# Kernel optimization log

Measured on AMD Instinct MI355X. Metric: run time of the kernel, lower is better.

## Reference

```python
import jax, jax.numpy as jnp
import numpy as np

B, LA, LB = 16, 2048, 2048
DA, DB, DH = 768, 512, 512
EPS = 1e-5


def _layer_norm(x, g, b):
    mu = jnp.mean(x, axis=-1, keepdims=True)
    var = jnp.var(x, axis=-1, keepdims=True)
    return (x - mu) * jax.lax.rsqrt(var + EPS) * g + b


def setup_inputs() -> dict:
    key = jax.random.key(0)
    ks = jax.random.split(key, 12)
    s = lambda d: 1.0 / np.sqrt(d)
    return {
        "z_a": jax.random.normal(ks[0], (B, LA, DA), jnp.float32),
        "z_b": jax.random.normal(ks[1], (B, LB, DB), jnp.float32),
        "Wa": jax.random.uniform(ks[2], (DA, DH), jnp.float32, -s(DA), s(DA)),
        "ba": jnp.zeros((DH,), jnp.float32),
        "Wb": jax.random.uniform(ks[3], (DB, DH), jnp.float32, -s(DB), s(DB)),
        "bb": jnp.zeros((DH,), jnp.float32),
        "W_co": jax.random.normal(ks[4], (DH, DH), jnp.float32),
        "Woa": jax.random.uniform(ks[5], (DH, DA), jnp.float32, -s(DH), s(DH)),
        "boa": jnp.zeros((DA,), jnp.float32),
        "Wob": jax.random.uniform(ks[6], (DH, DB), jnp.float32, -s(DH), s(DH)),
        "bob": jnp.zeros((DB,), jnp.float32),
        "ga": jnp.ones((DA,), jnp.float32),
        "beta_a": jnp.zeros((DA,), jnp.float32),
        "gb": jnp.ones((DB,), jnp.float32),
        "beta_b": jnp.zeros((DB,), jnp.float32),
    }


def reference(z_a, z_b, Wa, ba, Wb, bb, W_co, Woa, boa, Wob, bob, ga, beta_a, gb, beta_b):
    # projections to shared hidden space
    h_a = jnp.einsum('bld,dh->blh', z_a, Wa) + ba          # (B, LA, DH)
    h_b = jnp.einsum('bld,dh->blh', z_b, Wb) + bb          # (B, LB, DH)
    # bilinear tanh co-attention scores
    C = jnp.tanh(jnp.einsum('bih,hk,bjk->bij', h_a, W_co, h_b))  # (B, LA, LB)
    attn_a = jax.nn.softmax(C, axis=-1)                    # rows: over LB
    attn_b = jax.nn.softmax(C.transpose(0, 2, 1), axis=-1) # cols: over LA
    h_a_co = jnp.einsum('bij,bjh->bih', attn_a, h_b)       # (B, LA, DH)
    h_b_co = jnp.einsum('bji,bih->bjh', attn_b, h_a)       # (B, LB, DH)
    z_a_co = jnp.einsum('blh,hd->bld', h_a_co, Woa) + boa
    z_b_co = jnp.einsum('blh,hd->bld', h_b_co, Wob) + bob
    z_a_out = _layer_norm(z_a + z_a_co, ga, beta_a)
    z_b_out = _layer_norm(z_b + z_b_co, gb, beta_b)
    return (z_a_out, z_b_out)
```

## Files before the change

### kernel.cpp

```cpp
#include <hip/hip_runtime.h>
#include <stdint.h>

typedef short bf16x8 __attribute__((ext_vector_type(8)));
typedef float f32x16 __attribute__((ext_vector_type(16)));

#define BM 256
#define BN 256
#define BK 64
#define ABUF_U 16384
#define BUF_U  32768

#define AS1 __attribute__((address_space(1)))
#define AS3 __attribute__((address_space(3)))

__device__ __forceinline__ ushort f2bf(float x) {
    uint32_t u = __float_as_uint(x);
    u += 0x7FFFu + ((u >> 16) & 1u);
    return (ushort)(u >> 16);
}
__device__ __forceinline__ float bf2f(ushort u) {
    return __uint_as_float((uint)u << 16);
}

__device__ __forceinline__ void gload16(const void* g, void* l) {
    __builtin_amdgcn_global_load_lds((const AS1 void*)g, (AS3 void*)l, 16, 0, 0);
}

#define ISSUE2(kt, buf, i0)                                                          \
    do {                                                                             \
        gload16(((i0) < 4 ? Ap : Bp) + goff[i0] + (kt), smem + (buf)*BUF_U + loff[i0]); \
        gload16((((i0)+1) < 4 ? Ap : Bp) + goff[(i0)+1] + (kt), smem + (buf)*BUF_U + loff[(i0)+1]); \
    } while (0)

template<int MODE, bool HAS_BIAS, bool WRITE_T>
__global__ __launch_bounds__(512, 2)
void gemm_bt(const ushort* __restrict__ Aptr_, const ushort* __restrict__ Bptr_,
             void* __restrict__ Cptr_, ushort* __restrict__ CTptr_,
             const float* __restrict__ bias, const ushort* __restrict__ resid_,
             float* __restrict__ rsum_, float* __restrict__ csum_,
             const float* __restrict__ scale_,
             const ushort* __restrict__ Aptr2_, const ushort* __restrict__ Bptr2_,
             void* __restrict__ Cptr2_, const float* __restrict__ scale2_, int zsplit,
             int M, int N, int K, int lda, int ldb, int ldc,
             long sA, long sB, long sC, long sCT, long sSum,
             int ldct, int rbshift)
{
    extern __shared__ ushort smem[];

    const int gx = gridDim.x, gy = gridDim.y;
    const int nwg = gx * gy * (int)gridDim.z;
    int flat = ((int)blockIdx.z * gy + (int)blockIdx.y) * gx + (int)blockIdx.x;
    {
        const int q8 = nwg >> 3, r8 = nwg & 7;
        const int xcd = flat & 7, loc = flat >> 3;
        flat = (xcd < r8 ? xcd * (q8 + 1) : r8 * (q8 + 1) + (xcd - r8) * q8) + loc;
    }
    const int z   = flat / (gx * gy);
    const int rem = flat - z * (gx * gy);
    const int m0  = (rem % gx) * BM;
    const int n0  = (rem / gx) * BN;

    const bool sec = (z >= zsplit);
    const int  zl  = sec ? z - zsplit : z;

    const int tid  = threadIdx.x;
    const int lane = tid & 63;
    const int wave = tid >> 6;
    const int wr   = wave >> 2;
    const int wcn  = wave & 3;
    const int lr   = lane & 31, lh = lane >> 5;

    const ushort* Ap = (sec ? Aptr2_ : Aptr_) + (long)zl * sA;
    const ushort* Bp = (sec ? Bptr2_ : Bptr_) + (long)zl * sB;

    long goff[8]; int loff[8];
    #pragma unroll
    for (int u = 0; u < 4; ++u) {
        const int li  = u * 512 + tid;
        const int row = li >> 3;
        const int gck = (li & 7) ^ (row & 7);
        goff[u]     = (long)(m0 + row) * lda + gck * 8;
        loff[u]     = li * 8;
        goff[u + 4] = (long)(n0 + row) * ldb + gck * 8;
        loff[u + 4] = ABUF_U + li * 8;
    }

    f32x16 acc[4][2] = {};

    const int nk = K / BK;
    ISSUE2(0, 0, 0); ISSUE2(0, 0, 2); ISSUE2(0, 0, 4); ISSUE2(0, 0, 6);

    for (int t = 0; t < nk; ++t) {
        const int cur = t & 1, nxt = cur ^ 1;
        const ushort* As = smem + cur * BUF_U;
        const ushort* Bs = As + ABUF_U;
        const bool pf = (t + 1 < nk);
        const int kt1 = (t + 1) * BK;

        if (pf) {
            ISSUE2(kt1, nxt, 0);
            asm volatile("s_waitcnt vmcnt(2)" ::: "memory");
        } else {
            asm volatile("s_waitcnt vmcnt(0)" ::: "memory");
        }
        __builtin_amdgcn_s_barrier();

        #pragma unroll
        for (int kk = 0; kk < 4; ++kk) {
            bf16x8 af[4], bfv[2];
            #pragma unroll
            for (int tm = 0; tm < 4; ++tm) {
                const int row = wr * 128 + tm * 32 + lr;
                const int ck  = (kk * 2 + lh) ^ (row & 7);
                af[tm] = *(const bf16x8*)&As[row * BK + ck * 8];
            }
            #pragma unroll
            for (int tn = 0; tn < 2; ++tn) {
                const int row = wcn * 64 + tn * 32 + lr;
                const int ck  = (kk * 2 + lh) ^ (row & 7);
                bfv[tn] = *(const bf16x8*)&Bs[row * BK + ck * 8];
            }
            if (pf) {
                if (kk == 0)      ISSUE2(kt1, nxt, 2);
                else if (kk == 1) ISSUE2(kt1, nxt, 4);
                else if (kk == 2) ISSUE2(kt1, nxt, 6);
            }
            #pragma unroll
            for (int tm = 0; tm < 4; ++tm)
                #pragma unroll
                for (int tn = 0; tn < 2; ++tn)
                    acc[tm][tn] = __builtin_amdgcn_mfma_f32_32x32x16_bf16(
                        af[tm], bfv[tn], acc[tm][tn], 0, 0, 0);
        }

        asm volatile("s_waitcnt lgkmcnt(0)" ::: "memory");
        __builtin_amdgcn_s_barrier();
    }

    const int colb0 = n0 + wcn * 64 + lr;
    const int rowbw = m0 + wr * 128 + 4 * lh;

    if constexpr (MODE == 3) {
        ushort* Cp = (ushort*)Cptr_;
        #pragma unroll
        for (int tm = 0; tm < 4; ++tm)
            #pragma unroll
            for (int tn = 0; tn < 2; ++tn) {
                const int col = colb0 + tn * 32;
                const float bv = bias[col];
                #pragma unroll
                for (int q = 0; q < 4; ++q)
                    #pragma unroll
                    for (int s = 0; s < 4; ++s) {
                        const int row = rowbw + tm * 32 + q * 8 + s;
                        const long idx = (long)row * ldc + col;
                        Cp[idx] = f2bf(acc[tm][tn][q * 4 + s] + bv + bf2f(resid_[idx]));
                    }
            }
    } else if constexpr (MODE == 0) {
        ushort* Cp = (ushort*)Cptr_ + zl * sC;
        #pragma unroll
        for (int tm = 0; tm < 4; ++tm)
            #pragma unroll
            for (int tn = 0; tn < 2; ++tn) {
                const int col = colb0 + tn * 32;
                const float bv = HAS_BIAS ? bias[col] : 0.f;
                ushort us[16];
                #pragma unroll
                for (int rr = 0; rr < 16; ++rr) us[rr] = f2bf(acc[tm][tn][rr] + bv);
                #pragma unroll
                for (int q = 0; q < 4; ++q)
                    #pragma unroll
                    for (int s = 0; s < 4; ++s)
                        Cp[(long)(rowbw + tm * 32 + q * 8 + s) * ldc + col] = us[q * 4 + s];
                if constexpr (WRITE_T) {
                    #pragma unroll
                    for (int q = 0; q < 4; ++q) {
                        const int gr = rowbw + tm * 32 + q * 8;
                        const int bb = gr >> rbshift;
                        const int ii = gr & ((1 << rbshift) - 1);
                        *(ushort4*)&CTptr_[(long)bb * sCT + (long)col * ldct + ii] =
                            make_ushort4(us[q * 4 + 0], us[q * 4 + 1], us[q * 4 + 2], us[q * 4 + 3]);
                    }
                }
            }
    } else if constexpr (MODE == 1) {
        ushort* Ep  = (ushort*)Cptr_ + zl * sC;
        ushort* ETp = CTptr_ + zl * sCT;
        float* rs = rsum_ + zl * sSum;
        float* cs = csum_ + zl * sSum;
        float colp[2] = {0.f, 0.f};
        #pragma unroll
        for (int tm = 0; tm < 4; ++tm) {
            float rowp[16];
            #pragma unroll
            for (int rr = 0; rr < 16; ++rr) rowp[rr] = 0.f;
            #pragma unroll
            for (int tn = 0; tn < 2; ++tn) {
                const int col = colb0 + tn * 32;
                ushort us[16];
                #pragma unroll
                for (int rr = 0; rr < 16; ++rr) {
                    const float x  = acc[tm][tn][rr];
                    const float th = 1.f - 2.f / (__expf(2.f * x) + 1.f);
                    const float e  = __expf(th);
                    rowp[rr] += e;
                    colp[tn] += e;
                    us[rr] = f2bf(e);
                }
                #pragma unroll
                for (int q = 0; q < 4; ++q) {
                    #pragma unroll
                    for (int s = 0; s < 4; ++s)
                        Ep[(long)(rowbw + tm * 32 + q * 8 + s) * ldc + col] = us[q * 4 + s];
                    const int gr = rowbw + tm * 32 + q * 8;
                    *(ushort4*)&ETp[(long)col * ldct + gr] =
                        make_ushort4(us[q * 4 + 0], us[q * 4 + 1], us[q * 4 + 2], us[q * 4 + 3]);
                }
            }
            #pragma unroll
            for (int rr = 0; rr < 16; ++rr) {
                float v = rowp[rr];
                v += __shfl_xor(v, 1);  v += __shfl_xor(v, 2);
                v += __shfl_xor(v, 4);  v += __shfl_xor(v, 8);
                v += __shfl_xor(v, 16);
                if (lr == 0)
                    atomicAdd(&rs[rowbw + tm * 32 + (rr & 3) + 8 * (rr >> 2)], v);
            }
        }
        #pragma unroll
        for (int tn = 0; tn < 2; ++tn) {
            float v = colp[tn];
            v += __shfl_xor(v, 32);
            if (lh == 0) atomicAdd(&cs[colb0 + tn * 32], v);
        }
    } else {
        const float* sc = (sec ? scale2_ : scale_) + zl * sSum;
        ushort* Cp = (ushort*)(sec ? Cptr2_ : Cptr_) + zl * sC;
        #pragma unroll
        for (int tm = 0; tm < 4; ++tm) {
            float rcp[16];
            #pragma unroll
            for (int rr = 0; rr < 16; ++rr)
                rcp[rr] = 1.f / sc[rowbw + tm * 32 + (rr & 3) + 8 * (rr >> 2)];
            #pragma unroll
            for (int tn = 0; tn < 2; ++tn) {
                const int col = colb0 + tn * 32;
                #pragma unroll
                for (int q = 0; q < 4; ++q)
                    #pragma unroll
                    for (int s = 0; s < 4; ++s)
                        Cp[(long)(rowbw + tm * 32 + q * 8 + s) * ldc + col] =
                            f2bf(acc[tm][tn][q * 4 + s] * rcp[q * 4 + s]);
            }
        }
    }
}

__global__ __launch_bounds__(256)
void cast32to16(const float* __restrict__ in, ushort* __restrict__ out, long n) {
    const long stride = (long)gridDim.x * 256 * 8;
    for (long i = ((long)blockIdx.x * 256 + threadIdx.x) * 8; i < n; i += stride) {
        const float4 f0 = *(const float4*)(in + i);
        const float4 f1 = *(const float4*)(in + i + 4);
        uint4 w;
        w.x = (uint)f2bf(f0.x) | ((uint)f2bf(f0.y) << 16);
        w.y = (uint)f2bf(f0.z) | ((uint)f2bf(f0.w) << 16);
        w.z = (uint)f2bf(f1.x) | ((uint)f2bf(f1.y) << 16);
        w.w = (uint)f2bf(f1.z) | ((uint)f2bf(f1.w) << 16);
        *(uint4*)(out + i) = w;
    }
}

__global__ __launch_bounds__(256)
void tcast(const float* __restrict__ in, ushort* __restrict__ out, int R, int C) {
    __shared__ float t[32][33];
    const int bx = blockIdx.x * 32, by = blockIdx.y * 32;
    const int tx = threadIdx.x, ty = threadIdx.y;
    for (int i = ty; i < 32; i += 8) {
        const int r = by + i, cc = bx + tx;
        if (r < R && cc < C) t[i][tx] = in[(long)r * C + cc];
    }
    __syncthreads();
    for (int i = ty; i < 32; i += 8) {
        const int cc = bx + i, r = by + tx;
        if (cc < C && r < R) out[(long)cc * R + r] = f2bf(t[tx][i]);
    }
}

template<int D>
__global__ __launch_bounds__(D / 4)
void ln_bf(const ushort* __restrict__ y, float* __restrict__ out,
           const float* __restrict__ gam, const float* __restrict__ bet) {
    constexpr int NW = D / 256;
    const long row = blockIdx.x;
    const int tid = threadIdx.x;
    const ushort4 v4 = *(const ushort4*)&y[row * D + tid * 4];
    float v[4] = {bf2f(v4.x), bf2f(v4.y), bf2f(v4.z), bf2f(v4.w)};
    float s = v[0] + v[1] + v[2] + v[3];
    float s2 = v[0]*v[0] + v[1]*v[1] + v[2]*v[2] + v[3]*v[3];
    #pragma unroll
    for (int off = 1; off < 64; off <<= 1) {
        s  += __shfl_xor(s, off);
        s2 += __shfl_xor(s2, off);
    }
    __shared__ float ws[4], ws2[4];
    const int wave = tid >> 6, lane = tid & 63;
    if (lane == 0) { ws[wave] = s; ws2[wave] = s2; }
    __syncthreads();
    s = 0.f; s2 = 0.f;
    #pragma unroll
    for (int w2 = 0; w2 < NW; ++w2) { s += ws[w2]; s2 += ws2[w2]; }
    const float mu   = s / D;
    const float var  = s2 / D - mu * mu;
    const float rstd = rsqrtf(var + 1e-5f);
    const float4 gv = *(const float4*)&gam[tid * 4];
    const float4 bv = *(const float4*)&bet[tid * 4];
    float4 o;
    o.x = (v[0] - mu) * rstd * gv.x + bv.x;
    o.y = (v[1] - mu) * rstd * gv.y + bv.y;
    o.z = (v[2] - mu) * rstd * gv.z + bv.z;
    o.w = (v[3] - mu) * rstd * gv.w + bv.w;
    *(float4*)&out[row * D + tid * 4] = o;
}

extern "C" void kernel_launch(void* const* d_in, const int* in_sizes, int n_in,
                              void* d_out, int out_size, void* d_ws, size_t ws_size,
                              hipStream_t stream)
{
    (void)in_sizes; (void)n_in; (void)out_size; (void)ws_size;
    const float* z_a    = (const float*)d_in[0];
    const float* z_b    = (const float*)d_in[1];
    const float* Wa     = (const float*)d_in[2];
    const float* ba     = (const float*)d_in[3];
    const float* Wb     = (const float*)d_in[4];
    const float* bb     = (const float*)d_in[5];
    const float* Wco    = (const float*)d_in[6];
    const float* Woa    = (const float*)d_in[7];
    const float* boa    = (const float*)d_in[8];
    const float* Wob    = (const float*)d_in[9];
    const float* bob    = (const float*)d_in[10];
    const float* ga     = (const float*)d_in[11];
    const float* beta_a = (const float*)d_in[12];
    const float* gb     = (const float*)d_in[13];
    const float* beta_b = (const float*)d_in[14];

    const int Bn = 16, LA = 2048, LB = 2048, DA = 768, DB = 512, DH = 512;
    const int ZC = 8;
    const long MA = (long)Bn * LA;
    const long MB = (long)Bn * LB;

    char* w = (char*)d_ws;
    size_t off = 0;
    auto alc = [&](size_t bytes) { void* p = w + off; off += (bytes + 255) & ~(size_t)255; return p; };

    ushort* WaT  = (ushort*)alc((size_t)DH * DA * 2);
    ushort* WbT  = (ushort*)alc((size_t)DH * DB * 2);
    ushort* WcoT = (ushort*)alc((size_t)DH * DH * 2);
    ushort* WoaT = (ushort*)alc((size_t)DA * DH * 2);
    ushort* WobT = (ushort*)alc((size_t)DB * DH * 2);
    ushort* h_a  = (ushort*)alc((size_t)MA * DH * 2);
    ushort* h_b  = (ushort*)alc((size_t)MB * DH * 2);
    ushort* h_aT = (ushort*)alc((size_t)Bn * DH * LA * 2);
    ushort* h_bT = (ushort*)alc((size_t)Bn * DH * LB * 2);
    ushort* Ma   = (ushort*)alc((size_t)MA * DH * 2);
    ushort* E    = (ushort*)alc((size_t)ZC * LA * LB * 2);
    ushort* ET   = (ushort*)alc((size_t)ZC * LB * LA * 2);
    ushort* Pa   = (ushort*)alc((size_t)MA * DH * 2);
    ushort* Pb   = (ushort*)alc((size_t)MB * DH * 2);
    float*  rsum = (float*)alc((size_t)Bn * LA * 4);
    float*  csum = (float*)alc((size_t)Bn * LB * 4);

    ushort* za16 = (ushort*)d_out;
    ushort* zb16 = za16 + (size_t)MA * DA;
    ushort* yA = E;
    ushort* yB = ET;

    dim3 blk(512, 1, 1);
    dim3 blk256(256, 1, 1);
    dim3 tb(32, 8, 1);
    const int SHM = 2 * BUF_U * 2;
    const int NOSPLIT = 1 << 30;

    tcast<<<dim3(DH / 32, DA / 32, 1), tb, 0, stream>>>(Wa,  WaT,  DA, DH);
    tcast<<<dim3(DH / 32, DB / 32, 1), tb, 0, stream>>>(Wb,  WbT,  DB, DH);
    tcast<<<dim3(DH / 32, DH / 32, 1), tb, 0, stream>>>(Wco, WcoT, DH, DH);
    tcast<<<dim3(DA / 32, DH / 32, 1), tb, 0, stream>>>(Woa, WoaT, DH, DA);
    tcast<<<dim3(DB / 32, DH / 32, 1), tb, 0, stream>>>(Wob, WobT, DH, DB);

    cast32to16<<<dim3(2048, 1, 1), blk256, 0, stream>>>(z_a, za16, MA * DA);
    cast32to16<<<dim3(2048, 1, 1), blk256, 0, stream>>>(z_b, zb16, MB * DB);

    hipMemsetAsync(rsum, 0, (size_t)Bn * (LA + LB) * sizeof(float), stream);

    gemm_bt<0, true, true><<<dim3(MA / BM, DH / BN, 1), blk, SHM, stream>>>(
        za16, WaT, h_a, h_aT, ba, nullptr, nullptr, nullptr, nullptr,
        nullptr, nullptr, nullptr, nullptr, NOSPLIT,
        (int)MA, DH, DA, DA, DA, DH, 0, 0, 0, (long)DH * LA, 0, LA, 11);

    gemm_bt<0, true, true><<<dim3(MB / BM, DH / BN, 1), blk, SHM, stream>>>(
        zb16, WbT, h_b, h_bT, bb, nullptr, nullptr, nullptr, nullptr,
        nullptr, nullptr, nullptr, nullptr, NOSPLIT,
        (int)MB, DH, DB, DB, DB, DH, 0, 0, 0, (long)DH * LB, 0, LB, 11);

    gemm_bt<0, false, false><<<dim3(MA / BM, DH / BN, 1), blk, SHM, stream>>>(
        h_a, WcoT, Ma, nullptr, nullptr, nullptr, nullptr, nullptr, nullptr,
        nullptr, nullptr, nullptr, nullptr, NOSPLIT,
        (int)MA, DH, DH, DH, DH, DH, 0, 0, 0, 0, 0, 0, 0);

    for (int c = 0; c < Bn / ZC; ++c) {
        const ushort* Ma_c  = Ma   + (size_t)c * ZC * LA * DH;
        const ushort* hb_c  = h_b  + (size_t)c * ZC * LB * DH;
        const ushort* hbT_c = h_bT + (size_t)c * ZC * DH * LB;
        const ushort* haT_c = h_aT + (size_t)c * ZC * DH * LA;
        ushort* Pa_c = Pa + (size_t)c * ZC * LA * DH;
        ushort* Pb_c = Pb + (size_t)c * ZC * LB * DH;
        float* rs_c = rsum + (size_t)c * ZC * LA;
        float* cs_c = csum + (size_t)c * ZC * LB;

        gemm_bt<1, false, false><<<dim3(LA / BM, LB / BN, ZC), blk, SHM, stream>>>(
            Ma_c, hb_c, E, ET, nullptr, nullptr, rs_c, cs_c, nullptr,
            nullptr, nullptr, nullptr, nullptr, NOSPLIT,
            LA, LB, DH, DH, DH, LB,
            (long)LA * DH, (long)LB * DH, (long)LA * LB, (long)LB * LA, LA, LA, 0);

        gemm_bt<2, false, false><<<dim3(LA / BM, DH / BN, 2 * ZC), blk, SHM, stream>>>(
            E, hbT_c, Pa_c, nullptr, nullptr, nullptr, nullptr, nullptr, rs_c,
            ET, haT_c, Pb_c, cs_c, ZC,
            LA, DH, LB, LB, LB, DH,
            (long)LA * LB, (long)DH * LB, (long)LA * DH, 0, LA, 0, 0);
    }

    gemm_bt<3, true, false><<<dim3(MA / BM, DA / BN, 1), blk, SHM, stream>>>(
        Pa, WoaT, yA, nullptr, boa, za16, nullptr, nullptr, nullptr,
        nullptr, nullptr, nullptr, nullptr, NOSPLIT,
        (int)MA, DA, DH, DH, DH, DA, 0, 0, 0, 0, 0, 0, 0);

    gemm_bt<3, true, false><<<dim3(MB / BM, DB / BN, 1), blk, SHM, stream>>>(
        Pb, WobT, yB, nullptr, bob, zb16, nullptr, nullptr, nullptr,
        nullptr, nullptr, nullptr, nullptr, NOSPLIT,
        (int)MB, DB, DH, DH, DH, DB, 0, 0, 0, 0, 0, 0, 0);

    float* outA = (float*)d_out;
    float* outB = outA + MA * DA;
    ln_bf<768><<<dim3((unsigned)MA, 1, 1), dim3(192, 1, 1), 0, stream>>>(yA, outA, ga, beta_a);
    ln_bf<512><<<dim3((unsigned)MB, 1, 1), dim3(128, 1, 1), 0, stream>>>(yB, outB, gb, beta_b);
}
```

Before: 654.3 us.

## Reassociate B-side output projection before attention to drop the Pb GEMM

Computes G_b = h_a·Wob up front (written transposed only) and multiplies attn_b directly by it, so the B-side attention GEMM produces the output projection plus bias and residual in its epilogue. This removes the separate Pb→Wob GEMM and the h_aT transpose write, at the cost of one extra h_a×Wob GEMM of the same size. It relies on DB equalling DH so the existing grid shape for the mode-2 kernel still fits. Rounding changes because G_b is stored in bf16 before the attention weighting is applied.

```diff
diff --git a/kernel.cpp b/kernel.cpp
--- a/kernel.cpp
+++ b/kernel.cpp
@@ -32,7 +32,7 @@
         gload16((((i0)+1) < 4 ? Ap : Bp) + goff[(i0)+1] + (kt), smem + (buf)*BUF_U + loff[(i0)+1]); \
     } while (0)
 
-template<int MODE, bool HAS_BIAS, bool WRITE_T>
+template<int MODE, bool HAS_BIAS, bool WRITE_T, bool NO_C = false>
 __global__ __launch_bounds__(512, 2)
 void gemm_bt(const ushort* __restrict__ Aptr_, const ushort* __restrict__ Bptr_,
              void* __restrict__ Cptr_, ushort* __restrict__ CTptr_,
@@ -168,11 +168,13 @@
                 ushort us[16];
                 #pragma unroll
                 for (int rr = 0; rr < 16; ++rr) us[rr] = f2bf(acc[tm][tn][rr] + bv);
-                #pragma unroll
-                for (int q = 0; q < 4; ++q)
+                if constexpr (!NO_C) {
                     #pragma unroll
-                    for (int s = 0; s < 4; ++s)
-                        Cp[(long)(rowbw + tm * 32 + q * 8 + s) * ldc + col] = us[q * 4 + s];
+                    for (int q = 0; q < 4; ++q)
+                        #pragma unroll
+                        for (int s = 0; s < 4; ++s)
+                            Cp[(long)(rowbw + tm * 32 + q * 8 + s) * ldc + col] = us[q * 4 + s];
+                }
                 if constexpr (WRITE_T) {
                     #pragma unroll
                     for (int q = 0; q < 4; ++q) {
@@ -237,6 +239,7 @@
     } else {
         const float* sc = (sec ? scale2_ : scale_) + zl * sSum;
         ushort* Cp = (ushort*)(sec ? Cptr2_ : Cptr_) + zl * sC;
+        const ushort* Rp = (HAS_BIAS && sec) ? (resid_ + zl * sC) : nullptr;
         #pragma unroll
         for (int tm = 0; tm < 4; ++tm) {
             float rcp[16];
@@ -246,12 +249,17 @@
             #pragma unroll
             for (int tn = 0; tn < 2; ++tn) {
                 const int col = colb0 + tn * 32;
+                const float bv = (HAS_BIAS && sec) ? bias[col] : 0.f;
                 #pragma unroll
                 for (int q = 0; q < 4; ++q)
                     #pragma unroll
-                    for (int s = 0; s < 4; ++s)
-                        Cp[(long)(rowbw + tm * 32 + q * 8 + s) * ldc + col] =
-                            f2bf(acc[tm][tn][q * 4 + s] * rcp[q * 4 + s]);
+                    for (int s = 0; s < 4; ++s) {
+                        const int row = rowbw + tm * 32 + q * 8 + s;
+                        const long idx = (long)row * ldc + col;
+                        float v = acc[tm][tn][q * 4 + s] * rcp[q * 4 + s] + bv;
+                        if (Rp) v += bf2f(Rp[idx]);
+                        Cp[idx] = f2bf(v);
+                    }
             }
         }
     }
@@ -361,20 +369,19 @@
     ushort* WobT = (ushort*)alc((size_t)DB * DH * 2);
     ushort* h_a  = (ushort*)alc((size_t)MA * DH * 2);
     ushort* h_b  = (ushort*)alc((size_t)MB * DH * 2);
-    ushort* h_aT = (ushort*)alc((size_t)Bn * DH * LA * 2);
+    ushort* G_bT = (ushort*)alc((size_t)Bn * DB * LA * 2);
     ushort* h_bT = (ushort*)alc((size_t)Bn * DH * LB * 2);
     ushort* Ma   = (ushort*)alc((size_t)MA * DH * 2);
     ushort* E    = (ushort*)alc((size_t)ZC * LA * LB * 2);
     ushort* ET   = (ushort*)alc((size_t)ZC * LB * LA * 2);
     ushort* Pa   = (ushort*)alc((size_t)MA * DH * 2);
-    ushort* Pb   = (ushort*)alc((size_t)MB * DH * 2);
+    ushort* yB   = (ushort*)alc((size_t)MB * DB * 2);
     float*  rsum = (float*)alc((size_t)Bn * LA * 4);
     float*  csum = (float*)alc((size_t)Bn * LB * 4);
 
     ushort* za16 = (ushort*)d_out;
     ushort* zb16 = za16 + (size_t)MA * DA;
     ushort* yA = E;
-    ushort* yB = ET;
 
     dim3 blk(512, 1, 1);
     dim3 blk256(256, 1, 1);
@@ -393,10 +400,10 @@
 
     hipMemsetAsync(rsum, 0, (size_t)Bn * (LA + LB) * sizeof(float), stream);
 
-    gemm_bt<0, true, true><<<dim3(MA / BM, DH / BN, 1), blk, SHM, stream>>>(
-        za16, WaT, h_a, h_aT, ba, nullptr, nullptr, nullptr, nullptr,
+    gemm_bt<0, true, false><<<dim3(MA / BM, DH / BN, 1), blk, SHM, stream>>>(
+        za16, WaT, h_a, nullptr, ba, nullptr, nullptr, nullptr, nullptr,
         nullptr, nullptr, nullptr, nullptr, NOSPLIT,
-        (int)MA, DH, DA, DA, DA, DH, 0, 0, 0, (long)DH * LA, 0, LA, 11);
+        (int)MA, DH, DA, DA, DA, DH, 0, 0, 0, 0, 0, 0, 0);
 
     gemm_bt<0, true, true><<<dim3(MB / BM, DH / BN, 1), blk, SHM, stream>>>(
         zb16, WbT, h_b, h_bT, bb, nullptr, nullptr, nullptr, nullptr,
@@ -408,13 +415,19 @@
         nullptr, nullptr, nullptr, nullptr, NOSPLIT,
         (int)MA, DH, DH, DH, DH, DH, 0, 0, 0, 0, 0, 0, 0);
 
+    gemm_bt<0, false, true, true><<<dim3(MA / BM, DB / BN, 1), blk, SHM, stream>>>(
+        h_a, WobT, yB , G_bT, nullptr, nullptr, nullptr, nullptr, nullptr,
+        nullptr, nullptr, nullptr, nullptr, NOSPLIT,
+        (int)MA, DB, DH, DH, DH, DB, 0, 0, 0, (long)DB * LA, 0, LA, 11);
+
     for (int c = 0; c < Bn / ZC; ++c) {
         const ushort* Ma_c  = Ma   + (size_t)c * ZC * LA * DH;
         const ushort* hb_c  = h_b  + (size_t)c * ZC * LB * DH;
         const ushort* hbT_c = h_bT + (size_t)c * ZC * DH * LB;
-        const ushort* haT_c = h_aT + (size_t)c * ZC * DH * LA;
-        ushort* Pa_c = Pa + (size_t)c * ZC * LA * DH;
-        ushort* Pb_c = Pb + (size_t)c * ZC * LB * DH;
+        const ushort* GbT_c = G_bT + (size_t)c * ZC * DB * LA;
+        ushort* Pa_c  = Pa   + (size_t)c * ZC * LA * DH;
+        ushort* yB_c  = yB   + (size_t)c * ZC * LB * DB;
+        const ushort* zb_c = zb16 + (size_t)c * ZC * LB * DB;
         float* rs_c = rsum + (size_t)c * ZC * LA;
         float* cs_c = csum + (size_t)c * ZC * LB;
 
@@ -424,9 +437,9 @@
             LA, LB, DH, DH, DH, LB,
             (long)LA * DH, (long)LB * DH, (long)LA * LB, (long)LB * LA, LA, LA, 0);
 
-        gemm_bt<2, false, false><<<dim3(LA / BM, DH / BN, 2 * ZC), blk, SHM, stream>>>(
-            E, hbT_c, Pa_c, nullptr, nullptr, nullptr, nullptr, nullptr, rs_c,
-            ET, haT_c, Pb_c, cs_c, ZC,
+        gemm_bt<2, true, false><<<dim3(LA / BM, DH / BN, 2 * ZC), blk, SHM, stream>>>(
+            E, hbT_c, Pa_c, nullptr, bob, zb_c, nullptr, nullptr, rs_c,
+            ET, GbT_c, yB_c, cs_c, ZC,
             LA, DH, LB, LB, LB, DH,
             (long)LA * LB, (long)DH * LB, (long)LA * DH, 0, LA, 0, 0);
     }
@@ -436,11 +449,6 @@
         nullptr, nullptr, nullptr, nullptr, NOSPLIT,
         (int)MA, DA, DH, DH, DH, DA, 0, 0, 0, 0, 0, 0, 0);
 
-    gemm_bt<3, true, false><<<dim3(MB / BM, DB / BN, 1), blk, SHM, stream>>>(
-        Pb, WobT, yB, nullptr, bob, zb16, nullptr, nullptr, nullptr,
-        nullptr, nullptr, nullptr, nullptr, NOSPLIT,
-        (int)MB, DB, DH, DH, DH, DB, 0, 0, 0, 0, 0, 0, 0);
-
     float* outA = (float*)d_out;
     float* outB = outA + MA * DA;
     ln_bf<768><<<dim3((unsigned)MA, 1, 1), dim3(192, 1, 1), 0, stream>>>(yA, outA, ga, beta_a);
```

Measured after the change: 723.4 us. 10.6% more time.
